# Kernel tuning notes

Measured on AMD Instinct MI355X. Metric: run time of the kernel, lower is better.

Reference implementation:

```python
import jax, jax.numpy as jnp
import numpy as np

B, P, K, H, W = 32, 8, 17, 192, 192
ALPHA = 0.5
TEMP = 2.0
SIGMA = 3.0


def _bce_with_logits_mean(x, t):
    # numerically stable BCEWithLogitsLoss, reduction='mean'
    return jnp.mean(jnp.maximum(x, 0.0) - x * t + jnp.log1p(jnp.exp(-jnp.abs(x))))


def _kl_batchmean(s_logprob, t_prob):
    # torch KLDivLoss(reduction='batchmean'): sum(t * (log t - log s)) / batch
    return jnp.sum(t_prob * (jnp.log(t_prob) - s_logprob)) / s_logprob.shape[0]


def _keypoints_loss(pred, kps, vis):
    # pred: [B,K,H,W]; kps: [B,P,K,2] normalized; vis: [B,P,K] int
    b, k, h, w = pred.shape
    x = jnp.floor(kps[..., 0] * (w - 1))  # [B,P,K]; coords>=0 so floor == int()
    y = jnp.floor(kps[..., 1] * (h - 1))
    valid = ((vis > 0) & (x >= 0) & (x < w) & (y >= 0) & (y < h)).astype(pred.dtype)
    inv2s2 = 1.0 / (2.0 * SIGMA * SIGMA)
    ax = jnp.arange(w, dtype=pred.dtype)
    ay = jnp.arange(h, dtype=pred.dtype)
    # separable Gaussian: exp(-((a-x)^2+(b-y)^2)/2s^2) = gx(a)*gy(b)
    gx = jnp.exp(-(ax - x[..., None]) ** 2 * inv2s2) * valid[..., None]  # [B,P,K,W]
    gy = jnp.exp(-(ay - y[..., None]) ** 2 * inv2s2)                     # [B,P,K,H]
    # original indexes target[k][a,b] with a over grid_x (W axis); H==W required
    target = jnp.einsum('bpkw,bpkh->bkwh', gx, gy)  # [B,K,W,H] == [B,K,H,W]
    per = jnp.sum((pred - target) ** 2, axis=(1, 2, 3))          # F.mse_loss sum
    denom = jnp.sum(vis, axis=(1, 2)).astype(pred.dtype) + 1e-6
    return jnp.mean(per / denom)


def setup_inputs() -> dict:
    key = jax.random.key(0)
    k1, k2, k3, k4, k5, k6, k7 = jax.random.split(key, 7)
    return {
        's_seg_logits': jax.random.normal(k1, (B, 1, H, W), dtype=jnp.float32),
        's_pose_logits': jax.random.normal(k2, (B, K, H, W), dtype=jnp.float32),
        't_seg_logits': jax.random.normal(k3, (B, 1, H, W), dtype=jnp.float32),
        't_pose_logits': jax.random.normal(k4, (B, K, H, W), dtype=jnp.float32),
        'mask': jax.random.uniform(k5, (B, H, W), dtype=jnp.float32),
        'keypoints': jax.random.uniform(k6, (B, P, K, 2), dtype=jnp.float32),
        'visibilities': jax.random.randint(k7, (B, P, K), 0, 2, dtype=jnp.int32),
    }


def reference(s_seg_logits, s_pose_logits, t_seg_logits, t_pose_logits, mask, keypoints, visibilities):
    # task losses
    task_seg = _bce_with_logits_mean(s_seg_logits, mask[:, None])  # unsqueeze(1)
    task_pose = _keypoints_loss(s_pose_logits, keypoints, visibilities)
    task_loss = task_seg + task_pose
    # segmentation distillation (softmax over channel dim)
    s_seg_lp = jax.nn.log_softmax(s_seg_logits / TEMP, axis=1)
    t_seg_p = jax.nn.softmax(t_seg_logits / TEMP, axis=1)
    seg_distill = _kl_batchmean(s_seg_lp, t_seg_p) * TEMP ** 2
    # pose distillation (softmax over flattened K*H*W)
    s_pose_lp = jax.nn.log_softmax(s_pose_logits.reshape(s_pose_logits.shape[0], -1) / TEMP, axis=1)
    t_pose_p = jax.nn.softmax(t_pose_logits.reshape(t_pose_logits.shape[0], -1) / TEMP, axis=1)
    pose_distill = _kl_batchmean(s_pose_lp, t_pose_p) * TEMP ** 2
    distill_loss = seg_distill + pose_distill
    total = ALPHA * distill_loss + (1.0 - ALPHA) * task_loss
    return total
```

## Files before the change

### kernel.cpp

```cpp
#include <hip/hip_runtime.h>
#include <hip/hip_bf16.h>
#include <math.h>

#define B_   32
#define P_   8
#define K_   17
#define H_   192
#define W_   192
#define HW_  (H_*W_)
#define KP_SEG 3
#define BLK_PER_B (K_*KP_SEG)
#define KP_NBLK (B_*BLK_PER_B)
#define BCE_NBLK 96
#define TOTAL_BLK (KP_NBLK + BCE_NBLK)

#define WS_KP_OFF  0
#define WS_KL_OFF  2048
#define WS_BCE_OFF 8192

__device__ inline float wave_red_sum(float v) {
    for (int o = 32; o; o >>= 1) v += __shfl_xor(v, o, 64);
    return v;
}

__global__ void __launch_bounds__(256) main_kernel(
        const float* __restrict__ s_pose, const float* __restrict__ t_pose,
        const float* __restrict__ kps,    const int* __restrict__ vis,
        const float* __restrict__ s_seg,  const float* __restrict__ mask,
        float* __restrict__ ws) {
    __shared__ __align__(16) float gxs[P_][W_];
    __shared__ __align__(16) float gys[P_][H_];
    __shared__ float xk[P_], yk[P_], vld[P_];
    __shared__ float red[4][4];

    int blk = blockIdx.x;
    int tid = threadIdx.x;

    if (blk >= KP_NBLK) {
        int bidx = blk - KP_NBLK;
        const float4* x4 = (const float4*)s_seg;
        const float4* m4 = (const float4*)mask;
        size_t base = (size_t)bidx * 3072 + tid;
        float acc = 0.f;
#pragma unroll
        for (int j = 0; j < 12; j++) {
            float4 xv = x4[base + j*256];
            float4 tv = m4[base + j*256];
            acc += fmaxf(xv.x, 0.f) - xv.x*tv.x + log1pf(__expf(-fabsf(xv.x)));
            acc += fmaxf(xv.y, 0.f) - xv.y*tv.y + log1pf(__expf(-fabsf(xv.y)));
            acc += fmaxf(xv.z, 0.f) - xv.z*tv.z + log1pf(__expf(-fabsf(xv.z)));
            acc += fmaxf(xv.w, 0.f) - xv.w*tv.w + log1pf(__expf(-fabsf(xv.w)));
        }
        acc = wave_red_sum(acc);
        if ((tid & 63) == 0) red[0][tid >> 6] = acc;
        __syncthreads();
        if (tid == 0)
            ws[WS_BCE_OFF + bidx] = red[0][0] + red[0][1] + red[0][2] + red[0][3];
        return;
    }

    int b   = blk / BLK_PER_B;
    int r   = blk - b*BLK_PER_B;
    int k   = r / KP_SEG;
    int seg = r - k*KP_SEG;

    if (tid < P_) {
        int p = tid;
        float kx = kps[((b*P_ + p)*K_ + k)*2 + 0];
        float ky = kps[((b*P_ + p)*K_ + k)*2 + 1];
        int vv   = vis[(b*P_ + p)*K_ + k];
        float fx = floorf(kx * (float)(W_ - 1));
        float fy = floorf(ky * (float)(H_ - 1));
        bool ok = (vv > 0) && (fx >= 0.f) && (fx < (float)W_) && (fy >= 0.f) && (fy < (float)H_);
        xk[p] = fx; yk[p] = fy; vld[p] = ok ? 1.0f : 0.0f;
    }
    __syncthreads();

    const float inv2s2 = 1.0f / 18.0f;
    for (int e = tid; e < P_*W_; e += 256) {
        int p = e / W_;
        int i = e - p*W_;
        float dx = (float)i - xk[p];
        float dy = (float)i - yk[p];
        gxs[p][i] = __expf(-dx*dx*inv2s2) * vld[p];
        gys[p][i] = __expf(-dy*dy*inv2s2);
    }
    __syncthreads();

    const size_t off = (size_t)(b*K_ + k) * HW_;
    const float* pbase = s_pose + off;
    const float* tbase = t_pose + off;

    float mse = 0.f, Zu = 0.f, Zv = 0.f, A = 0.f;
#pragma unroll
    for (int it = 0; it < 3; it++) {
        int tau = it*256 + tid;
        int rg = tau / 48;
        int cg = tau - rg*48;
        int i0 = seg*64 + rg*4;
        int j0 = cg*4;
        float4 gx[P_], gy[P_];
#pragma unroll
        for (int p = 0; p < P_; p++) {
            gx[p] = *(const float4*)&gxs[p][i0];
            gy[p] = *(const float4*)&gys[p][j0];
        }
#pragma unroll
        for (int rr = 0; rr < 4; rr++) {
            const float* rowp = pbase + (i0 + rr)*W_ + j0;
            const float* rowt = tbase + (i0 + rr)*W_ + j0;
            float4 pv = *(const float4*)rowp;
            float4 tv = *(const float4*)rowt;
            float t0 = 0.f, t1 = 0.f, t2 = 0.f, t3 = 0.f;
#pragma unroll
            for (int p = 0; p < P_; p++) {
                float g = (rr == 0) ? gx[p].x : (rr == 1) ? gx[p].y : (rr == 2) ? gx[p].z : gx[p].w;
                t0 += g * gy[p].x;
                t1 += g * gy[p].y;
                t2 += g * gy[p].z;
                t3 += g * gy[p].w;
            }
            float d0 = pv.x - t0, d1 = pv.y - t1, d2 = pv.z - t2, d3 = pv.w - t3;
            mse += d0*d0 + d1*d1 + d2*d2 + d3*d3;
            {
                float u, v, eu;
                u = tv.x*0.5f; v = pv.x*0.5f; eu = __expf(u); Zu += eu; A += eu*(u - v); Zv += __expf(v);
                u = tv.y*0.5f; v = pv.y*0.5f; eu = __expf(u); Zu += eu; A += eu*(u - v); Zv += __expf(v);
                u = tv.z*0.5f; v = pv.z*0.5f; eu = __expf(u); Zu += eu; A += eu*(u - v); Zv += __expf(v);
                u = tv.w*0.5f; v = pv.w*0.5f; eu = __expf(u); Zu += eu; A += eu*(u - v); Zv += __expf(v);
            }
        }
    }

    mse = wave_red_sum(mse);
    Zu  = wave_red_sum(Zu);
    Zv  = wave_red_sum(Zv);
    A   = wave_red_sum(A);
    int w = tid >> 6;
    if ((tid & 63) == 0) {
        red[w][0] = mse; red[w][1] = Zu; red[w][2] = Zv; red[w][3] = A;
    }
    __syncthreads();
    if (tid == 0) {
        float m = 0.f, zu = 0.f, zv = 0.f, a = 0.f;
#pragma unroll
        for (int q = 0; q < 4; q++) {
            m += red[q][0]; zu += red[q][1]; zv += red[q][2]; a += red[q][3];
        }
        ws[WS_KP_OFF + blk] = m;
        float* o = ws + WS_KL_OFF + (size_t)blk * 3;
        o[0] = zu; o[1] = zv; o[2] = a;
    }
}

__global__ void __launch_bounds__(256) finalize_kernel(
        const float* __restrict__ ws, const int* __restrict__ vis,
        float* __restrict__ out) {
    __shared__ float rkp[B_][8], rzu[B_][8], rzv[B_][8], ra[B_][8];
    __shared__ int   rvs[B_][8];
    __shared__ float skl[B_], skp[B_];
    __shared__ float bw[4];
    int tid = threadIdx.x;
    int b = tid >> 3, s = tid & 7;

    float kp = 0.f, zu = 0.f, zv = 0.f, a = 0.f;
    for (int j = s; j < BLK_PER_B; j += 8) {
        int blk = b*BLK_PER_B + j;
        kp += ws[WS_KP_OFF + blk];
        const float* p = ws + WS_KL_OFF + (size_t)blk * 3;
        zu += p[0]; zv += p[1]; a += p[2];
    }
    int vs = 0;
    for (int m = s; m < P_*K_; m += 8) vs += vis[b*(P_*K_) + m];
    rkp[b][s] = kp; rzu[b][s] = zu; rzv[b][s] = zv; ra[b][s] = a; rvs[b][s] = vs;

    float bce = (tid < BCE_NBLK) ? ws[WS_BCE_OFF + tid] : 0.f;
    bce = wave_red_sum(bce);
    if ((tid & 63) == 0) bw[tid >> 6] = bce;
    __syncthreads();

    if (tid < B_) {
        float KP = 0.f, ZU = 0.f, ZV = 0.f, AA = 0.f; int VS = 0;
#pragma unroll
        for (int q = 0; q < 8; q++) {
            KP += rkp[tid][q]; ZU += rzu[tid][q]; ZV += rzv[tid][q];
            AA += ra[tid][q];  VS += rvs[tid][q];
        }
        skl[tid] = AA/ZU + (logf(ZV) - logf(ZU));
        skp[tid] = KP / ((float)VS + 1e-6f);
    }
    __syncthreads();

    if (tid == 0) {
        float kl = 0.f, kpv = 0.f;
        for (int i = 0; i < B_; i++) { kl += skl[i]; kpv += skp[i]; }
        float bsum = bw[0] + bw[1] + bw[2] + bw[3];
        float pose_distill = 4.0f * kl / (float)B_;
        float task_seg  = bsum / (float)(B_ * HW_);
        float task_pose = kpv / (float)B_;
        out[0] = 0.5f * pose_distill + 0.5f * (task_seg + task_pose);
    }
}

extern "C" void kernel_launch(void* const* d_in, const int* in_sizes, int n_in,
                              void* d_out, int out_size, void* d_ws, size_t ws_size,
                              hipStream_t stream) {
    const float* s_seg  = (const float*)d_in[0];
    const float* s_pose = (const float*)d_in[1];
    const float* t_pose = (const float*)d_in[3];
    const float* mask   = (const float*)d_in[4];
    const float* kps    = (const float*)d_in[5];
    const int*   vis    = (const int*)d_in[6];
    float* out = (float*)d_out;
    float* ws  = (float*)d_ws;

    main_kernel<<<TOTAL_BLK, 256, 0, stream>>>(s_pose, t_pose, kps, vis,
                                               s_seg, mask, ws);
    finalize_kernel<<<1, 256, 0, stream>>>(ws, vis, out);
}
```

Baseline: 208.4 us.

## Expand keypoint MSE algebraically into streamed sums and windowed Gaussian stamps

The squared error sum(p-t)^2 is rewritten as sum p^2 - 2·sum p·t + sum t^2. The full-tensor pass now only accumulates p^2 and the KL terms, so the dense 8-person Gaussian target is no longer built per pixel. The cross term is computed by per-keypoint blocks over a radius-18 window around each Gaussian. The t^2 term comes from separable closed-form 1D sums over person pairs. This removes the heavy per-pixel arithmetic and leaves the main pass limited by memory bandwidth, at the cost of possible fp32 cancellation and window truncation error.

```diff
diff --git a/kernel.cpp b/kernel.cpp
--- a/kernel.cpp
+++ b/kernel.cpp
@@ -1,5 +1,4 @@
 #include <hip/hip_runtime.h>
-#include <hip/hip_bf16.h>
 #include <math.h>
 
 #define B_   32
@@ -8,15 +7,25 @@
 #define H_   192
 #define W_   192
 #define HW_  (H_*W_)
-#define KP_SEG 3
-#define BLK_PER_B (K_*KP_SEG)
-#define KP_NBLK (B_*BLK_PER_B)
-#define BCE_NBLK 96
-#define TOTAL_BLK (KP_NBLK + BCE_NBLK)
-
-#define WS_KP_OFF  0
-#define WS_KL_OFF  2048
-#define WS_BCE_OFF 8192
+#define NBK  (B_*K_)
+
+#define STREAM_PER_B 153
+#define STREAM_BLKS  (B_*STREAM_PER_B)
+#define STAMP_BLKS   (B_*K_*P_)
+#define TSQ_BLKS     NBK
+#define BCE_BLKS     96
+#define STAMP_BASE   STREAM_BLKS
+#define TSQ_BASE     (STAMP_BASE+STAMP_BLKS)
+#define BCE_BASE     (TSQ_BASE+TSQ_BLKS)
+#define TOTAL_BLKS   (BCE_BASE+BCE_BLKS)
+
+#define RADIUS 18
+#define WIN    (2*RADIUS+1)
+
+#define WS_STREAM 0
+#define WS_STAMP  20480
+#define WS_TSQ    25088
+#define WS_BCE    25728
 
 __device__ inline float wave_red_sum(float v) {
     for (int o = 32; o; o >>= 1) v += __shfl_xor(v, o, 64);
@@ -28,21 +37,132 @@
         const float* __restrict__ kps,    const int* __restrict__ vis,
         const float* __restrict__ s_seg,  const float* __restrict__ mask,
         float* __restrict__ ws) {
-    __shared__ __align__(16) float gxs[P_][W_];
-    __shared__ __align__(16) float gys[P_][H_];
-    __shared__ float xk[P_], yk[P_], vld[P_];
-    __shared__ float red[4][4];
-
-    int blk = blockIdx.x;
-    int tid = threadIdx.x;
-
-    if (blk >= KP_NBLK) {
-        int bidx = blk - KP_NBLK;
+    __shared__ float sred[4][4];
+    __shared__ float gx_s[WIN + 3], gy_s[WIN + 3];
+
+    const int blk = blockIdx.x;
+    const int tid = threadIdx.x;
+    const float inv18 = 1.0f / 18.0f;
+
+    if (blk < STREAM_BLKS) {
+        int b = blk / STREAM_PER_B;
+        int r = blk - b*STREAM_PER_B;
+        const float4* s4 = (const float4*)s_pose + (size_t)b*(STREAM_PER_B*1024) + (size_t)r*1024;
+        const float4* t4 = (const float4*)t_pose + (size_t)b*(STREAM_PER_B*1024) + (size_t)r*1024;
+        float S2 = 0.f, Zu = 0.f, Zv = 0.f, A = 0.f;
+#pragma unroll
+        for (int j = 0; j < 4; j++) {
+            float4 sv = s4[j*256 + tid];
+            float4 tv = t4[j*256 + tid];
+            S2 += sv.x*sv.x + sv.y*sv.y + sv.z*sv.z + sv.w*sv.w;
+            float u0 = tv.x*0.5f, v0 = sv.x*0.5f;
+            float u1 = tv.y*0.5f, v1 = sv.y*0.5f;
+            float u2 = tv.z*0.5f, v2 = sv.z*0.5f;
+            float u3 = tv.w*0.5f, v3 = sv.w*0.5f;
+            float e0 = __expf(u0), e1 = __expf(u1), e2 = __expf(u2), e3 = __expf(u3);
+            Zu += (e0 + e1) + (e2 + e3);
+            A  += (e0*(u0-v0) + e1*(u1-v1)) + (e2*(u2-v2) + e3*(u3-v3));
+            Zv += (__expf(v0) + __expf(v1)) + (__expf(v2) + __expf(v3));
+        }
+        S2 = wave_red_sum(S2);
+        Zu = wave_red_sum(Zu);
+        Zv = wave_red_sum(Zv);
+        A  = wave_red_sum(A);
+        int w = tid >> 6;
+        if ((tid & 63) == 0) {
+            sred[w][0] = S2; sred[w][1] = Zu; sred[w][2] = Zv; sred[w][3] = A;
+        }
+        __syncthreads();
+        if (tid == 0) {
+            float* o = ws + WS_STREAM + (size_t)blk * 4;
+            o[0] = sred[0][0] + sred[1][0] + sred[2][0] + sred[3][0];
+            o[1] = sred[0][1] + sred[1][1] + sred[2][1] + sred[3][1];
+            o[2] = sred[0][2] + sred[1][2] + sred[2][2] + sred[3][2];
+            o[3] = sred[0][3] + sred[1][3] + sred[2][3] + sred[3][3];
+        }
+        return;
+    }
+
+    if (blk < TSQ_BASE) {
+        int sb  = blk - STAMP_BASE;
+        int b   = sb / (K_*P_);
+        int rem = sb - b*(K_*P_);
+        int k   = rem / P_;
+        int p   = rem - k*P_;
+        float kx = kps[((b*P_ + p)*K_ + k)*2 + 0];
+        float ky = kps[((b*P_ + p)*K_ + k)*2 + 1];
+        int   vv = vis[(b*P_ + p)*K_ + k];
+        float fx = floorf(kx * (float)(W_-1));
+        float fy = floorf(ky * (float)(H_-1));
+        bool ok = (vv > 0) && (fx >= 0.f) && (fx < (float)W_) && (fy >= 0.f) && (fy < (float)H_);
+        if (!ok) { if (tid == 0) ws[WS_STAMP + sb] = 0.f; return; }
+        int X0 = max(0, (int)fx - RADIUS), X1 = min(H_-1, (int)fx + RADIUS);
+        int Y0 = max(0, (int)fy - RADIUS), Y1 = min(W_-1, (int)fy + RADIUS);
+        int nr = X1 - X0 + 1, nc = Y1 - Y0 + 1;
+        if (tid < nr) {
+            float d = (float)(X0 + tid) - fx;
+            gx_s[tid] = __expf(-d*d*inv18);
+        } else if (tid >= 64 && tid - 64 < nc) {
+            float d = (float)(Y0 + tid - 64) - fy;
+            gy_s[tid - 64] = __expf(-d*d*inv18);
+        }
+        __syncthreads();
+        const float* pb = s_pose + (size_t)(b*K_ + k) * HW_;
+        float acc = 0.f;
+        int lim = nr << 6;
+        for (int e = tid; e < lim; e += 256) {
+            int row = e >> 6, col = e & 63;
+            if (col < nc)
+                acc += pb[(X0 + row)*W_ + (Y0 + col)] * gx_s[row] * gy_s[col];
+        }
+        acc = wave_red_sum(acc);
+        if ((tid & 63) == 0) sred[0][tid >> 6] = acc;
+        __syncthreads();
+        if (tid == 0)
+            ws[WS_STAMP + sb] = sred[0][0] + sred[0][1] + sred[0][2] + sred[0][3];
+        return;
+    }
+
+    if (blk < BCE_BASE) {
+        int sb = blk - TSQ_BASE;
+        int b = sb / K_, k = sb - b*K_;
+        int pq = tid >> 2, p = pq >> 3, q = pq & 7, ln = tid & 3;
+        float kxp = kps[((b*P_ + p)*K_ + k)*2 + 0];
+        float kyp = kps[((b*P_ + p)*K_ + k)*2 + 1];
+        float kxq = kps[((b*P_ + q)*K_ + k)*2 + 0];
+        float kyq = kps[((b*P_ + q)*K_ + k)*2 + 1];
+        int vp = vis[(b*P_ + p)*K_ + k];
+        int vq = vis[(b*P_ + q)*K_ + k];
+        float axp = floorf(kxp * 191.f), ayp = floorf(kyp * 191.f);
+        float axq = floorf(kxq * 191.f), ayq = floorf(kyq * 191.f);
+        bool okp = (vp > 0) && axp >= 0.f && axp < 192.f && ayp >= 0.f && ayp < 192.f;
+        bool okq = (vq > 0) && axq >= 0.f && axq < 192.f && ayq >= 0.f && ayq < 192.f;
+        float sx = 0.f, sy = 0.f;
+        int i0 = ln * 48;
+        for (int i = i0; i < i0 + 48; i++) {
+            float da = (float)i - axp, db = (float)i - axq;
+            sx += __expf(-(da*da + db*db)*inv18);
+            float ea = (float)i - ayp, eb = (float)i - ayq;
+            sy += __expf(-(ea*ea + eb*eb)*inv18);
+        }
+        sx += __shfl_xor(sx, 1, 64); sy += __shfl_xor(sy, 1, 64);
+        sx += __shfl_xor(sx, 2, 64); sy += __shfl_xor(sy, 2, 64);
+        float val = (ln == 0 && okp && okq) ? sx * sy : 0.f;
+        val = wave_red_sum(val);
+        if ((tid & 63) == 0) sred[0][tid >> 6] = val;
+        __syncthreads();
+        if (tid == 0)
+            ws[WS_TSQ + sb] = sred[0][0] + sred[0][1] + sred[0][2] + sred[0][3];
+        return;
+    }
+
+    {
+        int bidx = blk - BCE_BASE;
         const float4* x4 = (const float4*)s_seg;
         const float4* m4 = (const float4*)mask;
         size_t base = (size_t)bidx * 3072 + tid;
         float acc = 0.f;
-#pragma unroll
+#pragma unroll 4
         for (int j = 0; j < 12; j++) {
             float4 xv = x4[base + j*256];
             float4 tv = m4[base + j*256];
@@ -52,142 +172,52 @@
             acc += fmaxf(xv.w, 0.f) - xv.w*tv.w + log1pf(__expf(-fabsf(xv.w)));
         }
         acc = wave_red_sum(acc);
-        if ((tid & 63) == 0) red[0][tid >> 6] = acc;
+        if ((tid & 63) == 0) sred[0][tid >> 6] = acc;
         __syncthreads();
         if (tid == 0)
-            ws[WS_BCE_OFF + bidx] = red[0][0] + red[0][1] + red[0][2] + red[0][3];
-        return;
-    }
-
-    int b   = blk / BLK_PER_B;
-    int r   = blk - b*BLK_PER_B;
-    int k   = r / KP_SEG;
-    int seg = r - k*KP_SEG;
-
-    if (tid < P_) {
-        int p = tid;
-        float kx = kps[((b*P_ + p)*K_ + k)*2 + 0];
-        float ky = kps[((b*P_ + p)*K_ + k)*2 + 1];
-        int vv   = vis[(b*P_ + p)*K_ + k];
-        float fx = floorf(kx * (float)(W_ - 1));
-        float fy = floorf(ky * (float)(H_ - 1));
-        bool ok = (vv > 0) && (fx >= 0.f) && (fx < (float)W_) && (fy >= 0.f) && (fy < (float)H_);
-        xk[p] = fx; yk[p] = fy; vld[p] = ok ? 1.0f : 0.0f;
-    }
-    __syncthreads();
-
-    const float inv2s2 = 1.0f / 18.0f;
-    for (int e = tid; e < P_*W_; e += 256) {
-        int p = e / W_;
-        int i = e - p*W_;
-        float dx = (float)i - xk[p];
-        float dy = (float)i - yk[p];
-        gxs[p][i] = __expf(-dx*dx*inv2s2) * vld[p];
-        gys[p][i] = __expf(-dy*dy*inv2s2);
-    }
-    __syncthreads();
-
-    const size_t off = (size_t)(b*K_ + k) * HW_;
-    const float* pbase = s_pose + off;
-    const float* tbase = t_pose + off;
-
-    float mse = 0.f, Zu = 0.f, Zv = 0.f, A = 0.f;
-#pragma unroll
-    for (int it = 0; it < 3; it++) {
-        int tau = it*256 + tid;
-        int rg = tau / 48;
-        int cg = tau - rg*48;
-        int i0 = seg*64 + rg*4;
-        int j0 = cg*4;
-        float4 gx[P_], gy[P_];
-#pragma unroll
-        for (int p = 0; p < P_; p++) {
-            gx[p] = *(const float4*)&gxs[p][i0];
-            gy[p] = *(const float4*)&gys[p][j0];
-        }
-#pragma unroll
-        for (int rr = 0; rr < 4; rr++) {
-            const float* rowp = pbase + (i0 + rr)*W_ + j0;
-            const float* rowt = tbase + (i0 + rr)*W_ + j0;
-            float4 pv = *(const float4*)rowp;
-            float4 tv = *(const float4*)rowt;
-            float t0 = 0.f, t1 = 0.f, t2 = 0.f, t3 = 0.f;
-#pragma unroll
-            for (int p = 0; p < P_; p++) {
-                float g = (rr == 0) ? gx[p].x : (rr == 1) ? gx[p].y : (rr == 2) ? gx[p].z : gx[p].w;
-                t0 += g * gy[p].x;
-                t1 += g * gy[p].y;
-                t2 += g * gy[p].z;
-                t3 += g * gy[p].w;
-            }
-            float d0 = pv.x - t0, d1 = pv.y - t1, d2 = pv.z - t2, d3 = pv.w - t3;
-            mse += d0*d0 + d1*d1 + d2*d2 + d3*d3;
-            {
-                float u, v, eu;
-                u = tv.x*0.5f; v = pv.x*0.5f; eu = __expf(u); Zu += eu; A += eu*(u - v); Zv += __expf(v);
-                u = tv.y*0.5f; v = pv.y*0.5f; eu = __expf(u); Zu += eu; A += eu*(u - v); Zv += __expf(v);
-                u = tv.z*0.5f; v = pv.z*0.5f; eu = __expf(u); Zu += eu; A += eu*(u - v); Zv += __expf(v);
-                u = tv.w*0.5f; v = pv.w*0.5f; eu = __expf(u); Zu += eu; A += eu*(u - v); Zv += __expf(v);
-            }
-        }
-    }
-
-    mse = wave_red_sum(mse);
-    Zu  = wave_red_sum(Zu);
-    Zv  = wave_red_sum(Zv);
-    A   = wave_red_sum(A);
-    int w = tid >> 6;
-    if ((tid & 63) == 0) {
-        red[w][0] = mse; red[w][1] = Zu; red[w][2] = Zv; red[w][3] = A;
-    }
-    __syncthreads();
-    if (tid == 0) {
-        float m = 0.f, zu = 0.f, zv = 0.f, a = 0.f;
-#pragma unroll
-        for (int q = 0; q < 4; q++) {
-            m += red[q][0]; zu += red[q][1]; zv += red[q][2]; a += red[q][3];
-        }
-        ws[WS_KP_OFF + blk] = m;
-        float* o = ws + WS_KL_OFF + (size_t)blk * 3;
-        o[0] = zu; o[1] = zv; o[2] = a;
+            ws[WS_BCE + bidx] = sred[0][0] + sred[0][1] + sred[0][2] + sred[0][3];
     }
 }
 
 __global__ void __launch_bounds__(256) finalize_kernel(
         const float* __restrict__ ws, const int* __restrict__ vis,
         float* __restrict__ out) {
-    __shared__ float rkp[B_][8], rzu[B_][8], rzv[B_][8], ra[B_][8];
-    __shared__ int   rvs[B_][8];
+    __shared__ float rS2[B_][8], rZu[B_][8], rZv[B_][8], rA[B_][8];
+    __shared__ float rCr[B_][8], rTq[B_][8];
+    __shared__ int   rVs[B_][8];
     __shared__ float skl[B_], skp[B_];
     __shared__ float bw[4];
     int tid = threadIdx.x;
     int b = tid >> 3, s = tid & 7;
 
-    float kp = 0.f, zu = 0.f, zv = 0.f, a = 0.f;
-    for (int j = s; j < BLK_PER_B; j += 8) {
-        int blk = b*BLK_PER_B + j;
-        kp += ws[WS_KP_OFF + blk];
-        const float* p = ws + WS_KL_OFF + (size_t)blk * 3;
-        zu += p[0]; zv += p[1]; a += p[2];
-    }
+    float S2 = 0.f, Zu = 0.f, Zv = 0.f, A = 0.f, cr = 0.f, tq = 0.f;
+    for (int j = s; j < STREAM_PER_B; j += 8) {
+        const float* p = ws + WS_STREAM + (size_t)(b*STREAM_PER_B + j) * 4;
+        S2 += p[0]; Zu += p[1]; Zv += p[2]; A += p[3];
+    }
+    for (int j = s; j < K_*P_; j += 8) cr += ws[WS_STAMP + b*(K_*P_) + j];
+    for (int j = s; j < K_;    j += 8) tq += ws[WS_TSQ + b*K_ + j];
     int vs = 0;
     for (int m = s; m < P_*K_; m += 8) vs += vis[b*(P_*K_) + m];
-    rkp[b][s] = kp; rzu[b][s] = zu; rzv[b][s] = zv; ra[b][s] = a; rvs[b][s] = vs;
-
-    float bce = (tid < BCE_NBLK) ? ws[WS_BCE_OFF + tid] : 0.f;
+    rS2[b][s] = S2; rZu[b][s] = Zu; rZv[b][s] = Zv; rA[b][s] = A;
+    rCr[b][s] = cr; rTq[b][s] = tq; rVs[b][s] = vs;
+
+    float bce = (tid < BCE_BLKS) ? ws[WS_BCE + tid] : 0.f;
     bce = wave_red_sum(bce);
     if ((tid & 63) == 0) bw[tid >> 6] = bce;
     __syncthreads();
 
     if (tid < B_) {
-        float KP = 0.f, ZU = 0.f, ZV = 0.f, AA = 0.f; int VS = 0;
+        float tS2=0.f, tZu=0.f, tZv=0.f, tA=0.f, tCr=0.f, tTq=0.f; int tVs=0;
 #pragma unroll
-        for (int q = 0; q < 8; q++) {
-            KP += rkp[tid][q]; ZU += rzu[tid][q]; ZV += rzv[tid][q];
-            AA += ra[tid][q];  VS += rvs[tid][q];
-        }
-        skl[tid] = AA/ZU + (logf(ZV) - logf(ZU));
-        skp[tid] = KP / ((float)VS + 1e-6f);
+        for (int q2 = 0; q2 < 8; q2++) {
+            tS2 += rS2[tid][q2]; tZu += rZu[tid][q2]; tZv += rZv[tid][q2];
+            tA  += rA[tid][q2];  tCr += rCr[tid][q2]; tTq += rTq[tid][q2];
+            tVs += rVs[tid][q2];
+        }
+        float mse = tS2 - 2.f*tCr + tTq;
+        skl[tid] = tA/tZu + (logf(tZv) - logf(tZu));
+        skp[tid] = mse / ((float)tVs + 1e-6f);
     }
     __syncthreads();
 
@@ -214,7 +244,7 @@
     float* out = (float*)d_out;
     float* ws  = (float*)d_ws;
 
-    main_kernel<<<TOTAL_BLK, 256, 0, stream>>>(s_pose, t_pose, kps, vis,
-                                               s_seg, mask, ws);
+    main_kernel<<<TOTAL_BLKS, 256, 0, stream>>>(s_pose, t_pose, kps, vis,
+                                                s_seg, mask, ws);
     finalize_kernel<<<1, 256, 0, stream>>>(ws, vis, out);
 }
```

Result: slower. 228.1 us (+9.4%).
